# Kernel optimization log

Hardware: AMD Instinct MI355X
Metric: run time of the kernel (lower is better)

## Reference

```python
import jax, jax.numpy as jnp
import numpy as np
import math

B, S, D, H, F = 2, 2048, 1024, 16, 4096
DK = D // H
NEG_INF = -1000000000.0
EPS = 1e-5


def _layernorm(x, gamma, beta):
    # Faithful to source: torch.std default is unbiased (ddof=1), eps added to std
    mn = jnp.mean(x, axis=-1, keepdims=True)
    sd = jnp.std(x, axis=-1, keepdims=True, ddof=1)
    return (x - mn) / (sd + EPS) * gamma + beta


def _mha(xq, xkv, wq, bq, wk, bk, wv, bv, wo, bo, causal):
    b, sq, d = xq.shape
    sk = xkv.shape[1]
    q = (xq @ wq + bq).reshape(b, sq, H, DK).transpose(0, 2, 1, 3)   # [B,H,Sq,DK]
    k = (xkv @ wk + bk).reshape(b, sk, H, DK).transpose(0, 2, 1, 3)
    v = (xkv @ wv + bv).reshape(b, sk, H, DK).transpose(0, 2, 1, 3)
    scores = jnp.einsum('bhqd,bhkd->bhqk', q, k) / math.sqrt(DK)
    if causal:
        mask = jnp.triu(jnp.ones((sq, sk), dtype=scores.dtype), 1) * NEG_INF
        scores = scores + mask
    w = jax.nn.softmax(scores, axis=-1)
    att = jnp.einsum('bhqk,bhkd->bhqd', w, v).transpose(0, 2, 1, 3).reshape(b, sq, d)
    return att @ wo + bo


def setup_inputs() -> dict:
    key = jax.random.key(0)
    ks = jax.random.split(key, 32)
    it = iter(range(32))

    def lin(din, dout):
        kw = ks[next(it)]
        w = jax.random.normal(kw, (din, dout), jnp.float32) / math.sqrt(din)
        b = jnp.zeros((dout,), jnp.float32)
        return w, b

    X = jax.random.normal(ks[next(it)], (B, S, D), jnp.float32)
    y = jax.random.normal(ks[next(it)], (B, S, D), jnp.float32)
    wq1, bq1 = lin(D, D); wk1, bk1 = lin(D, D); wv1, bv1 = lin(D, D); wo1, bo1 = lin(D, D)
    wq2, bq2 = lin(D, D); wk2, bk2 = lin(D, D); wv2, bv2 = lin(D, D); wo2, bo2 = lin(D, D)
    wf1, bf1 = lin(D, F); wf2, bf2 = lin(F, D)
    g1 = jnp.ones((D,), jnp.float32); be1 = jnp.zeros((D,), jnp.float32)
    g2 = jnp.ones((D,), jnp.float32); be2 = jnp.zeros((D,), jnp.float32)
    g3 = jnp.ones((D,), jnp.float32); be3 = jnp.zeros((D,), jnp.float32)
    return dict(X=X, y=y,
                wq1=wq1, bq1=bq1, wk1=wk1, bk1=bk1, wv1=wv1, bv1=bv1, wo1=wo1, bo1=bo1,
                wq2=wq2, bq2=bq2, wk2=wk2, bk2=bk2, wv2=wv2, bv2=bv2, wo2=wo2, bo2=bo2,
                wf1=wf1, bf1=bf1, wf2=wf2, bf2=bf2,
                g1=g1, be1=be1, g2=g2, be2=be2, g3=g3, be3=be3)


def reference(X, y,
              wq1, bq1, wk1, bk1, wv1, bv1, wo1, bo1,
              wq2, bq2, wk2, bk2, wv2, bv2, wo2, bo2,
              wf1, bf1, wf2, bf2,
              g1, be1, g2, be2, g3, be3):
    # masked self-attention on decoder stream y (dropout = identity at inference)
    res = y
    out = _mha(y, y, wq1, bq1, wk1, bk1, wv1, bv1, wo1, bo1, causal=True)
    out = _layernorm(out + res, g1, be1)
    # cross-attention: queries from decoder, keys/values from encoder X
    res = out
    out = _mha(out, X, wq2, bq2, wk2, bk2, wv2, bv2, wo2, bo2, causal=False)
    out = _layernorm(out + res, g2, be2)
    # feed-forward (ReLU per intended semantics of the source)
    res = out
    out = jax.nn.relu(out @ wf1 + bf1) @ wf2 + bf2
    out = _layernorm(out + res, g3, be3)
    return out
```

## Files before the change

### kernel.cpp

```cpp
#include <hip/hip_runtime.h>

#define DEV __device__ __forceinline__

typedef __attribute__((ext_vector_type(8))) short short8;
typedef __attribute__((ext_vector_type(4))) short s16x4;
typedef __attribute__((ext_vector_type(4))) float f32x4;
typedef __attribute__((ext_vector_type(4))) unsigned u32x4;

DEV unsigned short f2b(float f){
  unsigned r;
  asm("v_cvt_pk_bf16_f32 %0, %1, %1" : "=v"(r) : "v"(f));
  return (unsigned short)r;
}
DEV unsigned cvt_pk2(float lo, float hi){
  unsigned r;
  asm("v_cvt_pk_bf16_f32 %0, %1, %2" : "=v"(r) : "v"(lo), "v"(hi));
  return r;
}
DEV float b2f(unsigned short u){ unsigned v = ((unsigned)u)<<16; float f; __builtin_memcpy(&f,&v,4); return f; }

DEV void gload_lds16(const void* g, void* l){
  __builtin_amdgcn_global_load_lds((const __attribute__((address_space(1))) void*)g,
                                   (__attribute__((address_space(3))) void*)l, 16, 0, 0);
}

#define SCL 0.18033688011112042f

__global__ __launch_bounds__(256) void cvt_f32_bf16(
    const float* __restrict__ in, unsigned short* __restrict__ out, int n)
{
  int i = (blockIdx.x*256 + threadIdx.x)*4;
  if (i >= n) return;
  float4 v = *(const float4*)(in + i);
  uint2 o;
  o.x = cvt_pk2(v.x, v.y);
  o.y = cvt_pk2(v.z, v.w);
  *(uint2*)(out + i) = o;
}

struct TransAll {
  const float* W[10]; unsigned short* Wt[10];
  int K[10], N[10], swapxy[10];
};
__global__ __launch_bounds__(256) void transpose_cvt_all(TransAll p)
{
  const int z = blockIdx.z;
  const int bx = p.swapxy[z] ? blockIdx.y : blockIdx.x;
  const int by = p.swapxy[z] ? blockIdx.x : blockIdx.y;
  const int K = p.K[z], N = p.N[z];
  const int n0 = bx*32, k0 = by*32;
  if (n0 >= N || k0 >= K) return;
  const float* __restrict__ W = p.W[z];
  unsigned short* __restrict__ Wt = p.Wt[z];
  __shared__ float tile[32][33];
  int tx = threadIdx.x & 31, ty = threadIdx.x >> 5;
  #pragma unroll
  for (int j=0;j<32;j+=8)
    tile[ty+j][tx] = W[(size_t)(k0+ty+j)*N + n0+tx];
  __syncthreads();
  #pragma unroll
  for (int j=0;j<32;j+=8)
    Wt[(size_t)(n0+ty+j)*K + k0+tx] = f2b(tile[tx][ty+j]);
}

template<int EPI>
__global__ __launch_bounds__(256) void gemm_bt(
    const unsigned short* __restrict__ A,
    const unsigned short* __restrict__ Bt,
    const float* __restrict__ bias,
    unsigned short* __restrict__ C,
    int M, int N, int Kc, int LDA, int LDB)
{
  __shared__ alignas(16) unsigned short Asm_[128*32];
  __shared__ alignas(16) unsigned short Bsm_[128*32];
  const int tid = threadIdx.x;
  const int wave = tid>>6, lane = tid&63;
  const int r0 = lane&15, kq = (lane>>4)*8, cq = lane>>4;
  const int m0 = blockIdx.y*128, n0 = blockIdx.x*128;
  const int wr = wave>>1, wc = wave&1;
  const int koff = blockIdx.z * Kc;
  const bool addb = (blockIdx.z == 0);
  C += (size_t)blockIdx.z * M * N;

  f32x4 zero4 = {0.f,0.f,0.f,0.f};
  f32x4 acc[4][4];
  #pragma unroll
  for (int m=0;m<4;m++)
    #pragma unroll
    for (int n=0;n<4;n++) acc[m][n]=zero4;

  const int nk = Kc>>5;
  for (int kt=0; kt<nk; kt++){
    #pragma unroll
    for (int i=0;i<2;i++){
      int idx = i*256 + tid;
      int row = idx>>2, kc = (idx&3)<<3;
      gload_lds16(A  + (size_t)(m0+row)*LDA + koff + (kt<<5) + kc,
                  Asm_ + (size_t)(i*256 + wave*64)*8);
      gload_lds16(Bt + (size_t)(n0+row)*LDB + koff + (kt<<5) + kc,
                  Bsm_ + (size_t)(i*256 + wave*64)*8);
    }
    __syncthreads();
    short8 a[4], b[4];
    #pragma unroll
    for (int m=0;m<4;m++) a[m] = *(const short8*)&Asm_[(wr*64 + m*16 + r0)*32 + kq];
    #pragma unroll
    for (int n=0;n<4;n++) b[n] = *(const short8*)&Bsm_[(wc*64 + n*16 + r0)*32 + kq];
    #pragma unroll
    for (int m=0;m<4;m++)
      #pragma unroll
      for (int n=0;n<4;n++)
        acc[m][n] = __builtin_amdgcn_mfma_f32_16x16x32_bf16(a[m], b[n], acc[m][n], 0,0,0);
    __syncthreads();
  }

  #pragma unroll
  for (int n=0;n<4;n++){
    int col = n0 + wc*64 + n*16 + r0;
    float bs = addb ? bias[col] : 0.f;
    #pragma unroll
    for (int m=0;m<4;m++){
      int rowb = m0 + wr*64 + m*16 + cq*4;
      #pragma unroll
      for (int reg=0;reg<4;reg++){
        float v = acc[m][n][reg] + bs;
        if (EPI==1) v = fmaxf(v, 0.f);
        C[(size_t)(rowb+reg)*N + col] = f2b(v);
      }
    }
  }
}

struct QKVArgs { const unsigned short* Aw[3]; const float* bias[3]; unsigned short* out[3]; };
__global__ __launch_bounds__(256) void gemm_qkv(
    const unsigned short* __restrict__ Bt,
    QKVArgs args, int M, int K)
{
  __shared__ alignas(16) unsigned short Asm_[128*32];
  __shared__ alignas(16) unsigned short Bsm_[128*32];
  const int tid = threadIdx.x;
  const int wave = tid>>6, lane = tid&63;
  const int r0 = lane&15, kq = (lane>>4)*8, cq = lane>>4;
  const int m0 = blockIdx.y*128, n0 = blockIdx.x*128;
  const int wr = wave>>1, wc = wave&1;
  const int which = n0>>10;
  const unsigned short* __restrict__ A = args.Aw[which];

  f32x4 zero4 = {0.f,0.f,0.f,0.f};
  f32x4 acc[4][4];
  #pragma unroll
  for (int m=0;m<4;m++)
    #pragma unroll
    for (int n=0;n<4;n++) acc[m][n]=zero4;

  const int nk = K>>5;
  for (int kt=0; kt<nk; kt++){
    #pragma unroll
    for (int i=0;i<2;i++){
      int idx = i*256 + tid;
      int row = idx>>2, kc = (idx&3)<<3;
      gload_lds16(A  + (size_t)(m0+row)*K + (kt<<5) + kc,
                  Asm_ + (size_t)(i*256 + wave*64)*8);
      gload_lds16(Bt + (size_t)(n0+row)*K + (kt<<5) + kc,
                  Bsm_ + (size_t)(i*256 + wave*64)*8);
    }
    __syncthreads();
    short8 a[4], b[4];
    #pragma unroll
    for (int m=0;m<4;m++) a[m] = *(const short8*)&Asm_[(wr*64 + m*16 + r0)*32 + kq];
    #pragma unroll
    for (int n=0;n<4;n++) b[n] = *(const short8*)&Bsm_[(wc*64 + n*16 + r0)*32 + kq];
    #pragma unroll
    for (int m=0;m<4;m++)
      #pragma unroll
      for (int n=0;n<4;n++)
        acc[m][n] = __builtin_amdgcn_mfma_f32_16x16x32_bf16(a[m], b[n], acc[m][n], 0,0,0);
    __syncthreads();
  }

  const int n0l = n0 & 1023;
  unsigned short* __restrict__ Cout = args.out[which];
  const float* __restrict__ bp = args.bias[which];
  const bool isV = (which == 2);
  const float scl = (which == 0) ? SCL : 1.f;

  #pragma unroll
  for (int n=0;n<4;n++){
    int col = n0l + wc*64 + n*16 + r0;
    float bs = bp[col];
    int h_ = col>>6, dk = col&63;
    #pragma unroll
    for (int m=0;m<4;m++){
      int rowb = m0 + wr*64 + m*16 + cq*4;
      #pragma unroll
      for (int reg=0;reg<4;reg++){
        float v = (acc[m][n][reg] + bs) * scl;
        int row = rowb + reg;
        int b_ = row>>11, s_ = row&2047;
        if (isV)
          Cout[(((size_t)(b_*16+h_))*64 + dk)*2048 + s_] = f2b(v);
        else
          Cout[(((size_t)(b_*16+h_))*2048 + s_)*64 + dk] = f2b(v);
      }
    }
  }
}

template<int MODE>
__global__ __launch_bounds__(256, 4) void attn_kernel(
    const unsigned short* __restrict__ Q,
    const unsigned short* __restrict__ K,
    const unsigned short* __restrict__ Vt,
    unsigned short* __restrict__ O,
    float* __restrict__ po, float* __restrict__ ml)
{
  __shared__ alignas(16) unsigned short Ksm[2][64*64];
  __shared__ alignas(16) unsigned short Vsm[2][64*64];
  const int S = 2048, DK = 64;
  const int h = blockIdx.y, b = blockIdx.z;
  const int tid = threadIdx.x, wave = tid>>6, lane = tid&63;
  const int r0 = lane&15, kq = (lane>>4)*8, cq = lane>>4;

  int qb, t0, t1, chunk = 0;
  bool partial = false;
  if (MODE==1){
    int bx = blockIdx.x;
    if (bx < 32){ qb = bx; t0 = 0; t1 = (qb<15?qb:15); chunk = 0; partial = (qb>=16); }
    else        { qb = bx-16; t0 = 16; t1 = qb; chunk = 1; partial = true; }
  } else { qb = blockIdx.x; t0 = 0; t1 = S/64 - 1; }

  const unsigned short* qh = Q  + ((size_t)(b*16+h))*S*DK;
  const unsigned short* kh = K  + ((size_t)(b*16+h))*S*DK;
  const unsigned short* vh = Vt + ((size_t)(b*16+h))*DK*S;

  const int idx0 = tid, idx1 = 256 + tid;
  const int rr0 = idx0>>3, cc0 = (idx0&7)<<3;
  const int rr1 = idx1>>3, cc1 = (idx1&7)<<3;
  const int sw0 = (idx0*8) ^ ((rr0&7)<<3);
  const int sw1 = (idx1*8) ^ ((rr1&7)<<3);
  const int swr = (r0&7)<<3;

  short8 qa[2];
  {
    int qrow = qb*64 + wave*16 + r0;
    qa[0] = *(const short8*)&qh[(size_t)qrow*DK + kq];
    qa[1] = *(const short8*)&qh[(size_t)qrow*DK + 32 + kq];
  }

  f32x4 zero4 = {0.f,0.f,0.f,0.f};
  f32x4 o[4];
  float mr = -INFINITY, lr = 0.f;
  #pragma unroll
  for (int n=0;n<4;n++) o[n]=zero4;

  short8 kr0, kr1, vr0, vr1;
  kr0 = *(const short8*)&kh[(size_t)(t0*64+rr0)*DK + cc0];
  kr1 = *(const short8*)&kh[(size_t)(t0*64+rr1)*DK + cc1];
  vr0 = *(const short8*)&vh[(size_t)rr0*S + t0*64 + cc0];
  vr1 = *(const short8*)&vh[(size_t)rr1*S + t0*64 + cc1];
  *(short8*)&Ksm[0][sw0] = kr0;
  *(short8*)&Ksm[0][sw1] = kr1;
  *(short8*)&Vsm[0][sw0] = vr0;
  *(short8*)&Vsm[0][sw1] = vr1;
  __syncthreads();

  int cur = 0;
  for (int t=t0; t<=t1; t++){
    const bool pf = (t < t1);
    if (pf){
      kr0 = *(const short8*)&kh[(size_t)((t+1)*64+rr0)*DK + cc0];
      kr1 = *(const short8*)&kh[(size_t)((t+1)*64+rr1)*DK + cc1];
      vr0 = *(const short8*)&vh[(size_t)rr0*S + (t+1)*64 + cc0];
      vr1 = *(const short8*)&vh[(size_t)rr1*S + (t+1)*64 + cc1];
    }

    f32x4 sv[4];
    #pragma unroll
    for (int n=0;n<4;n++) sv[n]=zero4;
    #pragma unroll
    for (int n=0;n<4;n++)
      #pragma unroll
      for (int kk=0;kk<2;kk++){
        short8 kb = *(const short8*)&Ksm[cur][(((n*16 + r0)*64) + kk*32 + kq) ^ swr];
        sv[n] = __builtin_amdgcn_mfma_f32_16x16x32_bf16(kb, qa[kk], sv[n], 0,0,0);
      }
    if (MODE==1 && t==qb){
      const int qg = wave*16 + r0;
      #pragma unroll
      for (int n=0;n<4;n++)
        #pragma unroll
        for (int reg=0;reg<4;reg++){
          if (n*16 + cq*4 + reg > qg) sv[n][reg] += -1000000000.0f;
        }
    }

    float m2 = fmaxf(fmaxf(fmaxf(sv[0][0],sv[0][1]),fmaxf(sv[0][2],sv[0][3])),
               fmaxf(fmaxf(fmaxf(sv[1][0],sv[1][1]),fmaxf(sv[1][2],sv[1][3])),
               fmaxf(fmaxf(fmaxf(sv[2][0],sv[2][1]),fmaxf(sv[2][2],sv[2][3])),
                     fmaxf(fmaxf(sv[3][0],sv[3][1]),fmaxf(sv[3][2],sv[3][3])))));
    m2 = fmaxf(m2, __shfl_xor(m2, 16, 64));
    m2 = fmaxf(m2, __shfl_xor(m2, 32, 64));
    bool need = (m2 > mr + 8.f);
    if (__ballot(need)){
      float nm = fmaxf(mr, m2);
      float fac = exp2f(mr - nm);
      mr = nm; lr *= fac;
      #pragma unroll
      for (int n=0;n<4;n++) o[n] *= fac;
    }
    float ps = 0.f;
    #pragma unroll
    for (int n=0;n<4;n++)
      #pragma unroll
      for (int reg=0;reg<4;reg++){
        float p = exp2f(sv[n][reg] - mr);
        sv[n][reg] = p; ps += p;
      }
    ps += __shfl_xor(ps, 16, 64);
    ps += __shfl_xor(ps, 32, 64);
    lr += ps;

    short8 pa[2];
    #pragma unroll
    for (int kk=0;kk<2;kk++){
      u32x4 w;
      w[0] = cvt_pk2(sv[2*kk][0],   sv[2*kk][1]);
      w[1] = cvt_pk2(sv[2*kk][2],   sv[2*kk][3]);
      w[2] = cvt_pk2(sv[2*kk+1][0], sv[2*kk+1][1]);
      w[3] = cvt_pk2(sv[2*kk+1][2], sv[2*kk+1][3]);
      pa[kk] = __builtin_bit_cast(short8, w);
    }

    #pragma unroll
    for (int n=0;n<4;n++)
      #pragma unroll
      for (int kk=0;kk<2;kk++){
        int base = (n*16 + r0)*64 + kk*32 + cq*4;
        s16x4 lo = *(const s16x4*)&Vsm[cur][base ^ swr];
        s16x4 hi = *(const s16x4*)&Vsm[cur][(base + 16) ^ swr];
        short8 vb = __builtin_shufflevector(lo, hi, 0,1,2,3,4,5,6,7);
        o[n] = __builtin_amdgcn_mfma_f32_16x16x32_bf16(vb, pa[kk], o[n], 0,0,0);
      }

    if (pf){
      *(short8*)&Ksm[cur^1][sw0] = kr0;
      *(short8*)&Ksm[cur^1][sw1] = kr1;
      *(short8*)&Vsm[cur^1][sw0] = vr0;
      *(short8*)&Vsm[cur^1][sw1] = vr1;
    }
    __syncthreads();
    cur ^= 1;
  }

  if (MODE==1 && partial){
    float* pop = po + (size_t)chunk*2097152;
    float* mlp = ml + (size_t)chunk*65536;
    const int bh = b*16 + h, qb16 = qb - 16;
    const int rowIdx = (bh*16 + qb16)*64 + wave*16 + r0;
    if (cq == 0){ mlp[rowIdx*2] = mr; mlp[rowIdx*2+1] = lr; }
    #pragma unroll
    for (int n=0;n<4;n++){
      float4 v; v.x=o[n][0]; v.y=o[n][1]; v.z=o[n][2]; v.w=o[n][3];
      *(float4*)&pop[(size_t)rowIdx*64 + n*16 + cq*4] = v;
    }
  } else {
    const int sg = qb*64 + wave*16 + r0;
    const float inv = 1.f / lr;
    unsigned short* op = O + ((size_t)b*S + sg)*1024 + h*64;
    #pragma unroll
    for (int n=0;n<4;n++){
      uint2 w;
      w.x = cvt_pk2(o[n][0]*inv, o[n][1]*inv);
      w.y = cvt_pk2(o[n][2]*inv, o[n][3]*inv);
      *(uint2*)(op + n*16 + cq*4) = w;
    }
  }
}

__global__ __launch_bounds__(256) void attn_merge(
    const float* __restrict__ po, const float* __restrict__ ml,
    unsigned short* __restrict__ O)
{
  int gid = blockIdx.x*256 + threadIdx.x;
  int row = gid>>4, dq = (gid&15)*4;
  float m0 = ml[row*2],          l0 = ml[row*2+1];
  float m1 = ml[65536 + row*2],  l1 = ml[65536 + row*2+1];
  float m = fmaxf(m0, m1);
  float a0 = exp2f(m0 - m), a1 = exp2f(m1 - m);
  float inv = 1.f / (l0*a0 + l1*a1);
  float4 v0 = *(const float4*)(po + (size_t)row*64 + dq);
  float4 v1 = *(const float4*)(po + 2097152 + (size_t)row*64 + dq);
  float r0 = (v0.x*a0 + v1.x*a1)*inv;
  float r1 = (v0.y*a0 + v1.y*a1)*inv;
  float r2 = (v0.z*a0 + v1.z*a1)*inv;
  float r3 = (v0.w*a0 + v1.w*a1)*inv;
  int bh = row>>10, qb16 = (row>>6)&15, qr = row&63;
  int b = bh>>4, h = bh&15;
  int s = (16+qb16)*64 + qr;
  unsigned short* op = O + ((size_t)b*2048 + s)*1024 + h*64 + dq;
  uint2 out; out.x = cvt_pk2(r0, r1); out.y = cvt_pk2(r2, r3);
  *(uint2*)op = out;
}

template<int OUT_F32>
__global__ __launch_bounds__(256) void add_ln3(
    const unsigned short* __restrict__ a0, const unsigned short* __restrict__ a1,
    const unsigned short* __restrict__ r,
    const float* __restrict__ g, const float* __restrict__ be, void* outp)
{
  const int row = blockIdx.x, tid = threadIdx.x;
  const size_t base = (size_t)row*1024 + tid*4;
  ushort4 va = *(const ushort4*)(a0 + base);
  ushort4 vb_ = *(const ushort4*)(a1 + base);
  ushort4 vr = *(const ushort4*)(r + base);
  float x[4];
  x[0] = b2f(va.x)+b2f(vb_.x)+b2f(vr.x);
  x[1] = b2f(va.y)+b2f(vb_.y)+b2f(vr.y);
  x[2] = b2f(va.z)+b2f(vb_.z)+b2f(vr.z);
  x[3] = b2f(va.w)+b2f(vb_.w)+b2f(vr.w);
  float s = x[0]+x[1]+x[2]+x[3];
  float ss = x[0]*x[0]+x[1]*x[1]+x[2]*x[2]+x[3]*x[3];
  #pragma unroll
  for (int d=1;d<64;d<<=1){ s += __shfl_xor(s,d,64); ss += __shfl_xor(ss,d,64); }
  __shared__ float rs[4], rss[4];
  int wave = tid>>6, lane = tid&63;
  if (lane==0){ rs[wave]=s; rss[wave]=ss; }
  __syncthreads();
  s = rs[0]+rs[1]+rs[2]+rs[3];
  ss = rss[0]+rss[1]+rss[2]+rss[3];
  float mean = s*(1.f/1024.f);
  float var = (ss - 1024.f*mean*mean)*(1.f/1023.f);
  float sd = sqrtf(fmaxf(var,0.f));
  float inv = 1.f/(sd + 1e-5f);
  float4 vg = *(const float4*)(g + tid*4);
  float4 vbe = *(const float4*)(be + tid*4);
  float o0 = (x[0]-mean)*inv*vg.x+vbe.x;
  float o1 = (x[1]-mean)*inv*vg.y+vbe.y;
  float o2 = (x[2]-mean)*inv*vg.z+vbe.z;
  float o3 = (x[3]-mean)*inv*vg.w+vbe.w;
  if (OUT_F32){
    float4 vo; vo.x=o0; vo.y=o1; vo.z=o2; vo.w=o3;
    *(float4*)((float*)outp + base) = vo;
  } else {
    uint2 vo; vo.x = cvt_pk2(o0,o1); vo.y = cvt_pk2(o2,o3);
    *(uint2*)((unsigned short*)outp + base) = vo;
  }
}

extern "C" void kernel_launch(void* const* d_in, const int* in_sizes, int n_in,
                              void* d_out, int out_size, void* d_ws, size_t ws_size,
                              hipStream_t stream)
{
  typedef const float* cf;
  cf X   = (cf)d_in[0],  y   = (cf)d_in[1];
  cf wq1 = (cf)d_in[2],  bq1 = (cf)d_in[3],  wk1 = (cf)d_in[4],  bk1 = (cf)d_in[5];
  cf wv1 = (cf)d_in[6],  bv1 = (cf)d_in[7],  wo1 = (cf)d_in[8],  bo1 = (cf)d_in[9];
  cf wq2 = (cf)d_in[10], bq2 = (cf)d_in[11], wk2 = (cf)d_in[12], bk2 = (cf)d_in[13];
  cf wv2 = (cf)d_in[14], bv2 = (cf)d_in[15], wo2 = (cf)d_in[16], bo2 = (cf)d_in[17];
  cf wf1 = (cf)d_in[18], bf1 = (cf)d_in[19], wf2 = (cf)d_in[20], bf2 = (cf)d_in[21];
  cf g1  = (cf)d_in[22], be1 = (cf)d_in[23], g2  = (cf)d_in[24], be2 = (cf)d_in[25];
  cf g3  = (cf)d_in[26], be3 = (cf)d_in[27];

  char* ws = (char*)d_ws;
  const size_t MB = 1u<<20;
  unsigned short* wq1t = (unsigned short*)(ws + 0*MB);
  unsigned short* wk1t = (unsigned short*)(ws + 2*MB);
  unsigned short* wv1t = (unsigned short*)(ws + 4*MB);
  unsigned short* wo1t = (unsigned short*)(ws + 6*MB);
  unsigned short* wq2t = (unsigned short*)(ws + 8*MB);
  unsigned short* wk2t = (unsigned short*)(ws + 10*MB);
  unsigned short* wv2t = (unsigned short*)(ws + 12*MB);
  unsigned short* wo2t = (unsigned short*)(ws + 14*MB);
  unsigned short* wf1t = (unsigned short*)(ws + 16*MB);
  unsigned short* wf2t = (unsigned short*)(ws + 24*MB);
  unsigned short* Qb   = (unsigned short*)(ws + 32*MB);
  unsigned short* Kb   = (unsigned short*)(ws + 40*MB);
  unsigned short* Vtb  = (unsigned short*)(ws + 48*MB);
  unsigned short* attno= (unsigned short*)(ws + 56*MB);
  unsigned short* hbuf = (unsigned short*)(ws + 32*MB);
  unsigned short* part = (unsigned short*)(ws + 64*MB);
  float*          poF  = (float*)(ws + 64*MB);
  float*          mlF  = (float*)(ws + 80*MB);
  unsigned short* x1b  = (unsigned short*)(ws + 80*MB);
  unsigned short* slot = (unsigned short*)(ws + 88*MB);
  unsigned short* yb = slot, *Xb = slot, *x2b = slot;

  dim3 blk(256);
  const int NTOK = 2*2048*1024;
  cvt_f32_bf16<<<NTOK/1024, blk, 0, stream>>>(y, yb, NTOK);

  {
    TransAll tp;
    const float* Ws[10]   = {wq1,wk1,wv1,wo1,wq2,wk2,wv2,wo2,wf1,wf2};
    unsigned short* Ts[10]= {wq1t,wk1t,wv1t,wo1t,wq2t,wk2t,wv2t,wo2t,wf1t,wf2t};
    for (int i=0;i<10;i++){
      tp.W[i]=Ws[i]; tp.Wt[i]=Ts[i];
      tp.K[i] = (i==9)?4096:1024;
      tp.N[i] = (i==8)?4096:1024;
      tp.swapxy[i] = (i==9)?1:0;
    }
    transpose_cvt_all<<<dim3(128,32,10), blk, 0, stream>>>(tp);
  }

  dim3 gqkv(24,32);
  dim3 gs(8,32,2);
  dim3 gff1(32,32,1);
  dim3 gac(48,16,2);
  dim3 gax(32,16,2);

  {
    QKVArgs a1;
    a1.Aw[0]=yb; a1.Aw[1]=yb; a1.Aw[2]=yb;
    a1.bias[0]=bq1; a1.bias[1]=bk1; a1.bias[2]=bv1;
    a1.out[0]=Qb; a1.out[1]=Kb; a1.out[2]=Vtb;
    gemm_qkv<<<gqkv, blk, 0, stream>>>(wq1t, a1, 4096, 1024);
  }
  attn_kernel<1><<<gac, blk, 0, stream>>>(Qb, Kb, Vtb, attno, poF, mlF);
  attn_merge<<<2048, blk, 0, stream>>>(poF, mlF, attno);
  gemm_bt<0><<<gs, blk, 0, stream>>>(attno, wo1t, bo1, part, 4096, 1024, 512, 1024, 1024);
  add_ln3<0><<<4096, blk, 0, stream>>>(part, part+4194304, yb, g1, be1, x1b);

  cvt_f32_bf16<<<NTOK/1024, blk, 0, stream>>>(X, Xb, NTOK);
  {
    QKVArgs a2;
    a2.Aw[0]=x1b; a2.Aw[1]=Xb; a2.Aw[2]=Xb;
    a2.bias[0]=bq2; a2.bias[1]=bk2; a2.bias[2]=bv2;
    a2.out[0]=Qb; a2.out[1]=Kb; a2.out[2]=Vtb;
    gemm_qkv<<<gqkv, blk, 0, stream>>>(wq2t, a2, 4096, 1024);
  }
  attn_kernel<0><<<gax, blk, 0, stream>>>(Qb, Kb, Vtb, attno, nullptr, nullptr);
  gemm_bt<0><<<gs, blk, 0, stream>>>(attno, wo2t, bo2, part, 4096, 1024, 512, 1024, 1024);
  add_ln3<0><<<4096, blk, 0, stream>>>(part, part+4194304, x1b, g2, be2, x2b);

  gemm_bt<1><<<gff1, blk, 0, stream>>>(x2b, wf1t, bf1, hbuf, 4096, 4096, 1024, 1024, 1024);
  gemm_bt<0><<<gs, blk, 0, stream>>>(hbuf, wf2t, bf2, part, 4096, 1024, 2048, 4096, 4096);
  add_ln3<1><<<4096, blk, 0, stream>>>(part, part+4194304, x2b, g3, be3, d_out);
}
```

Before: 432.4 us.

## Permute V layout for single 16B LDS reads and compute row sums via MFMA

The V-projection epilogue now writes V-transposed with a permuted sequence index inside each 32-element group. The attention kernel can then read each PV operand as one 16-byte LDS load instead of two 8-byte loads plus a shuffle. The softmax row sum is computed with two extra MFMAs against a ones vector, replacing the scalar accumulate and cross-lane shuffles. Global K/V prefetch addresses become incrementing pointers. The ones-MFMA sums the bf16-rounded probabilities, a slight numeric change, and any other reader of V must agree with the new permuted layout.

Result: no change. 425.7 us (-1.5%).

```diff
diff --git a/kernel.cpp b/kernel.cpp
--- a/kernel.cpp
+++ b/kernel.cpp
@@ -3,7 +3,6 @@
 #define DEV __device__ __forceinline__
 
 typedef __attribute__((ext_vector_type(8))) short short8;
-typedef __attribute__((ext_vector_type(4))) short s16x4;
 typedef __attribute__((ext_vector_type(4))) float f32x4;
 typedef __attribute__((ext_vector_type(4))) unsigned u32x4;
 
@@ -197,10 +196,12 @@
         float v = (acc[m][n][reg] + bs) * scl;
         int row = rowb + reg;
         int b_ = row>>11, s_ = row&2047;
-        if (isV)
-          Cout[(((size_t)(b_*16+h_))*64 + dk)*2048 + s_] = f2b(v);
-        else
+        if (isV){
+          int sp = (s_ & ~31) | (((s_>>2)&3)<<3) | (((s_>>4)&1)<<2) | (s_&3);
+          Cout[(((size_t)(b_*16+h_))*64 + dk)*2048 + sp] = f2b(v);
+        } else {
           Cout[(((size_t)(b_*16+h_))*2048 + s_)*64 + dk] = f2b(v);
+        }
       }
     }
   }
@@ -246,6 +247,9 @@
     qa[0] = *(const short8*)&qh[(size_t)qrow*DK + kq];
     qa[1] = *(const short8*)&qh[(size_t)qrow*DK + 32 + kq];
   }
+  short8 vones;
+  #pragma unroll
+  for (int j=0;j<8;j++) vones[j] = (short)0x3F80;
 
   f32x4 zero4 = {0.f,0.f,0.f,0.f};
   f32x4 o[4];
@@ -253,11 +257,16 @@
   #pragma unroll
   for (int n=0;n<4;n++) o[n]=zero4;
 
+  const unsigned short* kp0 = kh + (size_t)(t0*64+rr0)*DK + cc0;
+  const unsigned short* kp1 = kh + (size_t)(t0*64+rr1)*DK + cc1;
+  const unsigned short* vp0 = vh + (size_t)rr0*S + t0*64 + cc0;
+  const unsigned short* vp1 = vh + (size_t)rr1*S + t0*64 + cc1;
+
   short8 kr0, kr1, vr0, vr1;
-  kr0 = *(const short8*)&kh[(size_t)(t0*64+rr0)*DK + cc0];
-  kr1 = *(const short8*)&kh[(size_t)(t0*64+rr1)*DK + cc1];
-  vr0 = *(const short8*)&vh[(size_t)rr0*S + t0*64 + cc0];
-  vr1 = *(const short8*)&vh[(size_t)rr1*S + t0*64 + cc1];
+  kr0 = *(const short8*)kp0;
+  kr1 = *(const short8*)kp1;
+  vr0 = *(const short8*)vp0;
+  vr1 = *(const short8*)vp1;
   *(short8*)&Ksm[0][sw0] = kr0;
   *(short8*)&Ksm[0][sw1] = kr1;
   *(short8*)&Vsm[0][sw0] = vr0;
@@ -268,10 +277,11 @@
   for (int t=t0; t<=t1; t++){
     const bool pf = (t < t1);
     if (pf){
-      kr0 = *(const short8*)&kh[(size_t)((t+1)*64+rr0)*DK + cc0];
-      kr1 = *(const short8*)&kh[(size_t)((t+1)*64+rr1)*DK + cc1];
-      vr0 = *(const short8*)&vh[(size_t)rr0*S + (t+1)*64 + cc0];
-      vr1 = *(const short8*)&vh[(size_t)rr1*S + (t+1)*64 + cc1];
+      kp0 += 64*DK; kp1 += 64*DK; vp0 += 64; vp1 += 64;
+      kr0 = *(const short8*)kp0;
+      kr1 = *(const short8*)kp1;
+      vr0 = *(const short8*)vp0;
+      vr1 = *(const short8*)vp1;
     }
 
     f32x4 sv[4];
@@ -308,17 +318,11 @@
       #pragma unroll
       for (int n=0;n<4;n++) o[n] *= fac;
     }
-    float ps = 0.f;
     #pragma unroll
     for (int n=0;n<4;n++)
       #pragma unroll
-      for (int reg=0;reg<4;reg++){
-        float p = exp2f(sv[n][reg] - mr);
-        sv[n][reg] = p; ps += p;
-      }
-    ps += __shfl_xor(ps, 16, 64);
-    ps += __shfl_xor(ps, 32, 64);
-    lr += ps;
+      for (int reg=0;reg<4;reg++)
+        sv[n][reg] = exp2f(sv[n][reg] - mr);
 
     short8 pa[2];
     #pragma unroll
@@ -331,14 +335,18 @@
       pa[kk] = __builtin_bit_cast(short8, w);
     }
 
+    {
+      f32x4 ls = zero4;
+      ls = __builtin_amdgcn_mfma_f32_16x16x32_bf16(vones, pa[0], ls, 0,0,0);
+      ls = __builtin_amdgcn_mfma_f32_16x16x32_bf16(vones, pa[1], ls, 0,0,0);
+      lr += ls[0];
+    }
+
     #pragma unroll
     for (int n=0;n<4;n++)
       #pragma unroll
       for (int kk=0;kk<2;kk++){
-        int base = (n*16 + r0)*64 + kk*32 + cq*4;
-        s16x4 lo = *(const s16x4*)&Vsm[cur][base ^ swr];
-        s16x4 hi = *(const s16x4*)&Vsm[cur][(base + 16) ^ swr];
-        short8 vb = __builtin_shufflevector(lo, hi, 0,1,2,3,4,5,6,7);
+        short8 vb = *(const short8*)&Vsm[cur][(((n*16 + r0)*64) + kk*32 + cq*8) ^ swr];
         o[n] = __builtin_amdgcn_mfma_f32_16x16x32_bf16(vb, pa[kk], o[n], 0,0,0);
       }
 
```
